# Optimization experiments

Measured on AMD Instinct MI355X. Metric: run time of the kernel, lower is better.

The kernel has to match this reference:

```python
import jax, jax.numpy as jnp
import numpy as np

B, M, H = 8192, 512, 1024
CORRUPTION_LEN = int(0.6 * M)  # int(corruption_rate * input_dim)


def setup_inputs() -> dict:
    key = jax.random.key(0)
    ks = jax.random.split(key, 10)
    anchor = jax.random.normal(ks[0], (B, M), jnp.float32)
    random_sample = jax.random.normal(ks[1], (B, M), jnp.float32)
    # per-row random permutation -> exactly CORRUPTION_LEN corrupted features per row
    u = jax.random.uniform(ks[2], (B, M))
    ranks = jnp.argsort(jnp.argsort(u, axis=1), axis=1)  # rank of each column in a random permutation
    corruption_mask = ranks < CORRUPTION_LEN
    s_in = 1.0 / np.sqrt(M)
    s_h = 1.0 / np.sqrt(H)
    enc_w0 = jax.random.normal(ks[3], (M, H), jnp.float32) * s_in
    enc_b0 = jnp.full((H,), 0.01, jnp.float32)
    enc_w = jax.random.normal(ks[4], (3, H, H), jnp.float32) * s_h
    enc_b = jnp.full((3, H), 0.01, jnp.float32)
    head_w = jax.random.normal(ks[5], (2, H, H), jnp.float32) * s_h
    head_b = jnp.full((2, H), 0.01, jnp.float32)
    return {
        "anchor": anchor,
        "random_sample": random_sample,
        "corruption_mask": corruption_mask,
        "enc_w0": enc_w0,
        "enc_b0": enc_b0,
        "enc_w": enc_w,
        "enc_b": enc_b,
        "head_w": head_w,
        "head_b": head_b,
    }


def _mlp(x, w0, b0, ws, bs):
    # first dense + relu
    h = jax.nn.relu(x @ w0 + b0)
    # remaining dense + relu layers (small fixed count)
    for i in range(ws.shape[0]):
        h = jax.nn.relu(h @ ws[i] + bs[i])
    return h


def _embed(x, enc_w0, enc_b0, enc_w, enc_b, head_w, head_b):
    h = _mlp(x, enc_w0, enc_b0, enc_w, enc_b)          # encoder: 4 dense+relu
    h = jax.nn.relu(h @ head_w[0] + head_b[0])          # head: 2 dense+relu
    h = jax.nn.relu(h @ head_w[1] + head_b[1])
    return h


def reference(anchor, random_sample, corruption_mask, enc_w0, enc_b0, enc_w, enc_b, head_w, head_b):
    positive = jnp.where(corruption_mask, random_sample, anchor)
    emb_anchor = _embed(anchor, enc_w0, enc_b0, enc_w, enc_b, head_w, head_b)
    emb_positive = _embed(positive, enc_w0, enc_b0, enc_w, enc_b, head_w, head_b)
    return (emb_anchor, emb_positive)
```

## Files before the change

kernel.cpp:

```cpp
#include <hip/hip_runtime.h>
#include <hip/hip_bf16.h>
#include <stdint.h>


typedef __bf16 bf16x8 __attribute__((ext_vector_type(8)));
typedef float  f32x4  __attribute__((ext_vector_type(4)));

#define BM 128
#define BN 128
#define BK 64

__device__ __forceinline__ void gload_lds16(const void* g, void* l) {
  __builtin_amdgcn_global_load_lds(
      (const __attribute__((address_space(1))) uint32_t*)g,
      (__attribute__((address_space(3))) uint32_t*)l, 16, 0, 0);
}

__device__ __forceinline__ void fsplit(float v, uint16_t& ho, uint16_t& lo) {
  __bf16 hb = (__bf16)v;
  float  r  = v - (float)hb;
  __bf16 lb = (__bf16)r;
  ho = __builtin_bit_cast(uint16_t, hb);
  lo = __builtin_bit_cast(uint16_t, lb);
}

__global__ void detect_mask_kernel(const uint8_t* __restrict__ mask,
                                   int* __restrict__ flag) {
  if (threadIdx.x == 0 && blockIdx.x == 0) {
    uint32_t or_hi = 0;
    for (int i = 0; i < 1024; ++i)
      or_hi |= ((const uint32_t*)mask)[i] & 0xFFFFFF00u;
    *flag = (or_hi != 0) ? 1 : 0;
  }
}

__global__ void pack_kernel(const float* __restrict__ anchor,
                            const float* __restrict__ rnd,
                            const uint8_t* __restrict__ mask,
                            const int* __restrict__ mask_is_bytes,
                            uint16_t* __restrict__ Xhi, uint16_t* __restrict__ Xlo,
                            int total4) {
  int i = blockIdx.x * blockDim.x + threadIdx.x;
  if (i >= total4) return;
  float4 a = ((const float4*)anchor)[i];
  float4 r = ((const float4*)rnd)[i];
  const float* ap = (const float*)&a;
  const float* rp = (const float*)&r;
  uint32_t mbits;
  if (*mask_is_bytes) {
    uint32_t m = ((const uint32_t*)mask)[i];
    mbits = ((m >> 0) & 1u) | ((m >> 7) & 2u) | ((m >> 14) & 4u) | ((m >> 21) & 8u);
  } else {
    int4 mi = ((const int4*)mask)[i];
    mbits = (mi.x ? 1u : 0u) | (mi.y ? 2u : 0u) | (mi.z ? 4u : 0u) | (mi.w ? 8u : 0u);
  }
  ushort4 ah, al, ph, pl;
  uint16_t* ahp = (uint16_t*)&ah; uint16_t* alp = (uint16_t*)&al;
  uint16_t* php = (uint16_t*)&ph; uint16_t* plp = (uint16_t*)&pl;
#pragma unroll
  for (int j = 0; j < 4; ++j) {
    float av = ap[j];
    float pv = ((mbits >> j) & 1u) ? rp[j] : av;
    fsplit(av, ahp[j], alp[j]);
    fsplit(pv, php[j], plp[j]);
  }
  ((ushort4*)Xhi)[i] = ah;
  ((ushort4*)Xlo)[i] = al;
  ((ushort4*)Xhi)[i + total4] = ph;
  ((ushort4*)Xlo)[i + total4] = pl;
}

__global__ void wprep_kernel(const float* __restrict__ W,
                             uint16_t* __restrict__ Wh, uint16_t* __restrict__ Wl,
                             int K, int N) {
  __shared__ float t[32][33];
  int k0 = blockIdx.x * 32, n0 = blockIdx.y * 32;
  int tr = threadIdx.x >> 5, tc = threadIdx.x & 31;
#pragma unroll
  for (int i = 0; i < 4; ++i)
    t[tr + i * 8][tc] = W[(size_t)(k0 + tr + i * 8) * N + n0 + tc];
  __syncthreads();
#pragma unroll
  for (int i = 0; i < 4; ++i) {
    int n = tr + i * 8;
    float v = t[tc][n];
    uint16_t h, l;
    fsplit(v, h, l);
    size_t o = (size_t)(n0 + n) * K + k0 + tc;
    Wh[o] = h; Wl[o] = l;
  }
}

template <int K, bool LAST>
__global__ __launch_bounds__(256, 2) void gemm_kernel(
    const uint16_t* __restrict__ Ah, const uint16_t* __restrict__ Al,
    const uint16_t* __restrict__ Bh, const uint16_t* __restrict__ Bl,
    const float* __restrict__ bias,
    uint16_t* __restrict__ Yh, uint16_t* __restrict__ Yl,
    float* __restrict__ Yf) {
  __shared__ uint16_t sAh[BM * BK], sAl[BM * BK], sBh[BN * BK], sBl[BN * BK];

  int bid = blockIdx.x;
  int swz = (bid & 7) * 128 + (bid >> 3);
  int tn = swz & 7;
  int tm = swz >> 3;
  const int brow = tm * BM, bcol = tn * BN;

  const int tid = threadIdx.x;
  const int w = tid >> 6, l = tid & 63;
  const int wr = w >> 1, wc = w & 1;
  const int lr = l >> 3, lc = (l & 7) * 8;

  f32x4 acc[4][4];
#pragma unroll
  for (int m = 0; m < 4; ++m)
#pragma unroll
    for (int n = 0; n < 4; ++n) acc[m][n] = 0;

  for (int k0 = 0; k0 < K; k0 += BK) {
#pragma unroll
    for (int t = 0; t < 4; ++t) {
      int r = w * 32 + t * 8;
      size_t ga = (size_t)(brow + r + lr) * K + k0 + lc;
      size_t gb = (size_t)(bcol + r + lr) * K + k0 + lc;
      gload_lds16(Ah + ga, &sAh[r * BK]);
      gload_lds16(Al + ga, &sAl[r * BK]);
      gload_lds16(Bh + gb, &sBh[r * BK]);
      gload_lds16(Bl + gb, &sBl[r * BK]);
    }
    __syncthreads();

#pragma unroll
    for (int kk = 0; kk < 2; ++kk) {
      const int ko = kk * 32 + (l >> 4) * 8;
      bf16x8 aH[4], aL[4], bH[4], bL[4];
#pragma unroll
      for (int m = 0; m < 4; ++m) {
        int row = wr * 64 + m * 16 + (l & 15);
        aH[m] = *(const bf16x8*)&sAh[row * BK + ko];
        aL[m] = *(const bf16x8*)&sAl[row * BK + ko];
      }
#pragma unroll
      for (int n = 0; n < 4; ++n) {
        int col = wc * 64 + n * 16 + (l & 15);
        bH[n] = *(const bf16x8*)&sBh[col * BK + ko];
        bL[n] = *(const bf16x8*)&sBl[col * BK + ko];
      }
#pragma unroll
      for (int m = 0; m < 4; ++m)
#pragma unroll
        for (int n = 0; n < 4; ++n) {
          acc[m][n] = __builtin_amdgcn_mfma_f32_16x16x32_bf16(aH[m], bH[n], acc[m][n], 0, 0, 0);
          acc[m][n] = __builtin_amdgcn_mfma_f32_16x16x32_bf16(aH[m], bL[n], acc[m][n], 0, 0, 0);
          acc[m][n] = __builtin_amdgcn_mfma_f32_16x16x32_bf16(aL[m], bH[n], acc[m][n], 0, 0, 0);
        }
    }
    __syncthreads();
  }

  float bb[4];
#pragma unroll
  for (int n = 0; n < 4; ++n) bb[n] = bias[bcol + wc * 64 + n * 16 + (l & 15)];
#pragma unroll
  for (int m = 0; m < 4; ++m) {
#pragma unroll
    for (int j = 0; j < 4; ++j) {
      int row = brow + wr * 64 + m * 16 + (l >> 4) * 4 + j;
#pragma unroll
      for (int n = 0; n < 4; ++n) {
        int col = bcol + wc * 64 + n * 16 + (l & 15);
        float v = acc[m][n][j] + bb[n];
        v = v > 0.f ? v : 0.f;
        size_t o = (size_t)row * 1024 + col;
        if (LAST) {
          Yf[o] = v;
        } else {
          uint16_t h, lo2;
          fsplit(v, h, lo2);
          Yh[o] = h; Yl[o] = lo2;
        }
      }
    }
  }
}

extern "C" void kernel_launch(void* const* d_in, const int* in_sizes, int n_in,
                              void* d_out, int out_size, void* d_ws, size_t ws_size,
                              hipStream_t stream) {
  (void)in_sizes; (void)n_in; (void)out_size; (void)ws_size;
  const float*   anchor = (const float*)d_in[0];
  const float*   rnd    = (const float*)d_in[1];
  const uint8_t* mask   = (const uint8_t*)d_in[2];
  const float*   enc_w0 = (const float*)d_in[3];
  const float*   enc_b0 = (const float*)d_in[4];
  const float*   enc_w  = (const float*)d_in[5];
  const float*   enc_b  = (const float*)d_in[6];
  const float*   head_w = (const float*)d_in[7];
  const float*   head_b = (const float*)d_in[8];
  float* out = (float*)d_out;

  const int B = 8192, M = 512;
  const size_t W_ELEMS = (size_t)512 * 1024 + 5ull * 1024 * 1024;

  uint16_t* WT_H = (uint16_t*)d_ws;
  uint16_t* WT_L = WT_H + W_ELEMS;
  uint16_t* X0_H = WT_L + W_ELEMS;
  uint16_t* X0_L = X0_H + (size_t)16384 * 512;
  uint16_t* Y_H  = X0_L + (size_t)16384 * 512;
  uint16_t* Y_L  = Y_H + (size_t)16384 * 1024;
  int* mflag     = (int*)(Y_L + (size_t)16384 * 1024);
  uint16_t* Z_H = (uint16_t*)d_out;
  uint16_t* Z_L = Z_H + (size_t)16384 * 1024;

  detect_mask_kernel<<<1, 64, 0, stream>>>(mask, mflag);

  int total4 = B * M / 4;
  pack_kernel<<<total4 / 256, 256, 0, stream>>>(anchor, rnd, mask, mflag, X0_H, X0_L, total4);

  const size_t WOFF[6] = {0, 524288, 1572864, 2621440, 3670016, 4718592};
  wprep_kernel<<<dim3(16, 32), 256, 0, stream>>>(enc_w0, WT_H + WOFF[0], WT_L + WOFF[0], 512, 1024);
  for (int i = 0; i < 3; ++i)
    wprep_kernel<<<dim3(32, 32), 256, 0, stream>>>(enc_w + (size_t)i * 1048576,
                                                   WT_H + WOFF[1 + i], WT_L + WOFF[1 + i], 1024, 1024);
  for (int i = 0; i < 2; ++i)
    wprep_kernel<<<dim3(32, 32), 256, 0, stream>>>(head_w + (size_t)i * 1048576,
                                                   WT_H + WOFF[4 + i], WT_L + WOFF[4 + i], 1024, 1024);

  dim3 g(1024), b(256);
  gemm_kernel<512,  false><<<g, b, 0, stream>>>(X0_H, X0_L, WT_H + WOFF[0], WT_L + WOFF[0], enc_b0,        Y_H, Y_L, nullptr);
  gemm_kernel<1024, false><<<g, b, 0, stream>>>(Y_H,  Y_L,  WT_H + WOFF[1], WT_L + WOFF[1], enc_b,         Z_H, Z_L, nullptr);
  gemm_kernel<1024, false><<<g, b, 0, stream>>>(Z_H,  Z_L,  WT_H + WOFF[2], WT_L + WOFF[2], enc_b + 1024,  Y_H, Y_L, nullptr);
  gemm_kernel<1024, false><<<g, b, 0, stream>>>(Y_H,  Y_L,  WT_H + WOFF[3], WT_L + WOFF[3], enc_b + 2048,  Z_H, Z_L, nullptr);
  gemm_kernel<1024, false><<<g, b, 0, stream>>>(Z_H,  Z_L,  WT_H + WOFF[4], WT_L + WOFF[4], head_b,        Y_H, Y_L, nullptr);
  gemm_kernel<1024, true ><<<g, b, 0, stream>>>(Y_H,  Y_L,  WT_H + WOFF[5], WT_L + WOFF[5], head_b + 1024, nullptr, nullptr, out);
}
```

Before: 666.1 us.

## Rewrite split-bf16 GEMM with 256x256 tiles, interleaved swizzled layout, double buffering

Repacks activations and weights into one interleaved hi/lo operand buffer with an XOR-swizzled 32-wide K-group layout, so a single row read serves both halves without LDS bank conflicts. The GEMM moves to 256x256 tiles with 512 threads and 8 waves, a double-buffered LDS pipeline that prefetches the next K-group while MFMAs run, manual waitcnt/barrier scheduling and setprio. Larger tiles cut global traffic per FLOP and the prefetch hides load latency. The cost is higher register and LDS pressure (128 KB LDS per block, which may limit occupancy to one block per CU) and a narrower mask-detect scan.

```diff
diff --git a/kernel.cpp b/kernel.cpp
--- a/kernel.cpp
+++ b/kernel.cpp
@@ -5,10 +5,7 @@
 
 typedef __bf16 bf16x8 __attribute__((ext_vector_type(8)));
 typedef float  f32x4  __attribute__((ext_vector_type(4)));
-
-#define BM 128
-#define BN 128
-#define BK 64
+typedef unsigned short u16x8 __attribute__((ext_vector_type(8)));
 
 __device__ __forceinline__ void gload_lds16(const void* g, void* l) {
   __builtin_amdgcn_global_load_lds(
@@ -28,7 +25,7 @@
                                    int* __restrict__ flag) {
   if (threadIdx.x == 0 && blockIdx.x == 0) {
     uint32_t or_hi = 0;
-    for (int i = 0; i < 1024; ++i)
+    for (int i = 0; i < 256; ++i)
       or_hi |= ((const uint32_t*)mask)[i] & 0xFFFFFF00u;
     *flag = (or_hi != 0) ? 1 : 0;
   }
@@ -38,150 +35,244 @@
                             const float* __restrict__ rnd,
                             const uint8_t* __restrict__ mask,
                             const int* __restrict__ mask_is_bytes,
-                            uint16_t* __restrict__ Xhi, uint16_t* __restrict__ Xlo,
-                            int total4) {
-  int i = blockIdx.x * blockDim.x + threadIdx.x;
-  if (i >= total4) return;
-  float4 a = ((const float4*)anchor)[i];
-  float4 r = ((const float4*)rnd)[i];
-  const float* ap = (const float*)&a;
-  const float* rp = (const float*)&r;
-  uint32_t mbits;
+                            uint16_t* __restrict__ Xop) {
+  int t = blockIdx.x * 256 + threadIdx.x;
+  int row = t >> 6;
+  int idx = t & 63;
+  int g = idx >> 2, c = idx & 3;
+  int kbase = idx * 8;
+  const float4* ap = (const float4*)(anchor + (size_t)row * 512 + kbase);
+  const float4* rp = (const float4*)(rnd + (size_t)row * 512 + kbase);
+  float a[8], r[8];
+  *(float4*)&a[0] = ap[0]; *(float4*)&a[4] = ap[1];
+  *(float4*)&r[0] = rp[0]; *(float4*)&r[4] = rp[1];
+  uint32_t mb;
   if (*mask_is_bytes) {
-    uint32_t m = ((const uint32_t*)mask)[i];
-    mbits = ((m >> 0) & 1u) | ((m >> 7) & 2u) | ((m >> 14) & 4u) | ((m >> 21) & 8u);
+    const uint32_t* mp = (const uint32_t*)(mask + (size_t)row * 512 + kbase);
+    uint32_t w0 = mp[0], w1 = mp[1];
+    mb = 0;
+#pragma unroll
+    for (int j = 0; j < 4; ++j) {
+      mb |= ((w0 >> (8 * j)) & 1u) << j;
+      mb |= ((w1 >> (8 * j)) & 1u) << (4 + j);
+    }
   } else {
-    int4 mi = ((const int4*)mask)[i];
-    mbits = (mi.x ? 1u : 0u) | (mi.y ? 2u : 0u) | (mi.z ? 4u : 0u) | (mi.w ? 8u : 0u);
-  }
-  ushort4 ah, al, ph, pl;
-  uint16_t* ahp = (uint16_t*)&ah; uint16_t* alp = (uint16_t*)&al;
-  uint16_t* php = (uint16_t*)&ph; uint16_t* plp = (uint16_t*)&pl;
-#pragma unroll
-  for (int j = 0; j < 4; ++j) {
-    float av = ap[j];
-    float pv = ((mbits >> j) & 1u) ? rp[j] : av;
-    fsplit(av, ahp[j], alp[j]);
-    fsplit(pv, php[j], plp[j]);
-  }
-  ((ushort4*)Xhi)[i] = ah;
-  ((ushort4*)Xlo)[i] = al;
-  ((ushort4*)Xhi)[i + total4] = ph;
-  ((ushort4*)Xlo)[i + total4] = pl;
+    const int* mi = (const int*)mask + (size_t)row * 512 + kbase;
+    int4 m0 = ((const int4*)mi)[0], m1 = ((const int4*)mi)[1];
+    mb = (m0.x ? 1u : 0) | (m0.y ? 2u : 0) | (m0.z ? 4u : 0) | (m0.w ? 8u : 0) |
+         (m1.x ? 16u : 0) | (m1.y ? 32u : 0) | (m1.z ? 64u : 0) | (m1.w ? 128u : 0);
+  }
+  u16x8 ah, al, ph, pl;
+#pragma unroll
+  for (int j = 0; j < 8; ++j) {
+    uint16_t h, lo;
+    fsplit(a[j], h, lo); ah[j] = h; al[j] = lo;
+    float pv = ((mb >> j) & 1u) ? r[j] : a[j];
+    fsplit(pv, h, lo); ph[j] = h; pl[j] = lo;
+  }
+  int s = row & 7;
+  size_t base = ((size_t)row * 16 + g) * 64;
+  *(u16x8*)(Xop + base + (size_t)((c ^ s)) * 8) = ah;
+  *(u16x8*)(Xop + base + (size_t)(((c + 4) ^ s)) * 8) = al;
+  size_t pbase = ((size_t)(row + 8192) * 16 + g) * 64;
+  *(u16x8*)(Xop + pbase + (size_t)((c ^ s)) * 8) = ph;
+  *(u16x8*)(Xop + pbase + (size_t)(((c + 4) ^ s)) * 8) = pl;
 }
 
 __global__ void wprep_kernel(const float* __restrict__ W,
-                             uint16_t* __restrict__ Wh, uint16_t* __restrict__ Wl,
-                             int K, int N) {
-  __shared__ float t[32][33];
-  int k0 = blockIdx.x * 32, n0 = blockIdx.y * 32;
-  int tr = threadIdx.x >> 5, tc = threadIdx.x & 31;
+                             uint16_t* __restrict__ Bop, int K) {
+  __shared__ float tbuf[32][33];
+  int g = blockIdx.x, n0 = blockIdx.y * 32;
+  int tid = threadIdx.x;
 #pragma unroll
   for (int i = 0; i < 4; ++i)
-    t[tr + i * 8][tc] = W[(size_t)(k0 + tr + i * 8) * N + n0 + tc];
+    tbuf[(tid >> 5) + i * 8][tid & 31] =
+        W[((size_t)g * 32 + (tid >> 5) + i * 8) * 1024 + n0 + (tid & 31)];
   __syncthreads();
-#pragma unroll
-  for (int i = 0; i < 4; ++i) {
-    int n = tr + i * 8;
-    float v = t[tc][n];
-    uint16_t h, l;
-    fsplit(v, h, l);
-    size_t o = (size_t)(n0 + n) * K + k0 + tc;
-    Wh[o] = h; Wl[o] = l;
+  if (tid < 128) {
+    int nl = tid >> 2, c = tid & 3;
+    int n = n0 + nl, s = n & 7;
+    u16x8 hi, lo;
+#pragma unroll
+    for (int j = 0; j < 8; ++j) {
+      uint16_t h, l2;
+      fsplit(tbuf[c * 8 + j][nl], h, l2);
+      hi[j] = h; lo[j] = l2;
+    }
+    size_t base = ((size_t)n * (K / 32) + g) * 64;
+    *(u16x8*)(Bop + base + (size_t)((c ^ s)) * 8) = hi;
+    *(u16x8*)(Bop + base + (size_t)(((c + 4) ^ s)) * 8) = lo;
+  }
+}
+
+__device__ __forceinline__ void mfma_row(f32x4* accrow, bf16x8 aH, bf16x8 aL,
+                                         const bf16x8* bh, const bf16x8* bl) {
+#pragma unroll
+  for (int n = 0; n < 4; ++n) {
+    accrow[n] = __builtin_amdgcn_mfma_f32_16x16x32_bf16(aH, bh[n], accrow[n], 0, 0, 0);
+    accrow[n] = __builtin_amdgcn_mfma_f32_16x16x32_bf16(aH, bl[n], accrow[n], 0, 0, 0);
+    accrow[n] = __builtin_amdgcn_mfma_f32_16x16x32_bf16(aL, bh[n], accrow[n], 0, 0, 0);
   }
 }
 
 template <int K, bool LAST>
-__global__ __launch_bounds__(256, 2) void gemm_kernel(
-    const uint16_t* __restrict__ Ah, const uint16_t* __restrict__ Al,
-    const uint16_t* __restrict__ Bh, const uint16_t* __restrict__ Bl,
+__global__ __launch_bounds__(512, 2) void gemm_kernel(
+    const uint16_t* __restrict__ Aop, const uint16_t* __restrict__ Bop,
     const float* __restrict__ bias,
-    uint16_t* __restrict__ Yh, uint16_t* __restrict__ Yl,
-    float* __restrict__ Yf) {
-  __shared__ uint16_t sAh[BM * BK], sAl[BM * BK], sBh[BN * BK], sBl[BN * BK];
+    uint16_t* __restrict__ Yop, float* __restrict__ Yf) {
+  constexpr int KG = K / 32;
+  __shared__ uint16_t sA[2][256 * 64];
+  __shared__ uint16_t sB[2][256 * 64];
 
   int bid = blockIdx.x;
-  int swz = (bid & 7) * 128 + (bid >> 3);
-  int tn = swz & 7;
-  int tm = swz >> 3;
-  const int brow = tm * BM, bcol = tn * BN;
+  int xcd = bid & 7, lid = bid >> 3;
+  int tm = xcd * 8 + (lid >> 2), tn = lid & 3;
+  const int brow = tm * 256, bcol = tn * 256;
 
   const int tid = threadIdx.x;
-  const int w = tid >> 6, l = tid & 63;
-  const int wr = w >> 1, wc = w & 1;
-  const int lr = l >> 3, lc = (l & 7) * 8;
-
-  f32x4 acc[4][4];
-#pragma unroll
-  for (int m = 0; m < 4; ++m)
+  const int l = tid & 63, w = tid >> 6;
+  const int wr = w >> 2, wc = w & 3;
+  const int l15 = l & 15, c16 = l >> 4;
+
+  f32x4 acc[8][4];
+#pragma unroll
+  for (int m = 0; m < 8; ++m)
 #pragma unroll
     for (int n = 0; n < 4; ++n) acc[m][n] = 0;
 
-  for (int k0 = 0; k0 < K; k0 += BK) {
-#pragma unroll
-    for (int t = 0; t < 4; ++t) {
-      int r = w * 32 + t * 8;
-      size_t ga = (size_t)(brow + r + lr) * K + k0 + lc;
-      size_t gb = (size_t)(bcol + r + lr) * K + k0 + lc;
-      gload_lds16(Ah + ga, &sAh[r * BK]);
-      gload_lds16(Al + ga, &sAl[r * BK]);
-      gload_lds16(Bh + gb, &sBh[r * BK]);
-      gload_lds16(Bl + gb, &sBl[r * BK]);
+#define STAGE_A(g_, buf_)                                                     \
+  _Pragma("unroll") for (int i = 0; i < 4; ++i) {                             \
+    int row_ = i * 64 + (tid >> 3);                                           \
+    gload_lds16(Aop + ((size_t)(brow + row_) * KG + (g_)) * 64 + (tid & 7) * 8,\
+                &sA[buf_][i * 4096 + tid * 8]);                               \
+  }
+#define STAGE_B(g_, buf_)                                                     \
+  _Pragma("unroll") for (int i = 0; i < 4; ++i) {                             \
+    int row_ = i * 64 + (tid >> 3);                                           \
+    gload_lds16(Bop + ((size_t)(bcol + row_) * KG + (g_)) * 64 + (tid & 7) * 8,\
+                &sB[buf_][i * 4096 + tid * 8]);                               \
+  }
+#define READ_A(mm, aH, aL)                                                    \
+  {                                                                           \
+    int fr_ = wr * 128 + (mm)*16 + l15;                                       \
+    const uint16_t* rp_ = pA + fr_ * 64;                                      \
+    aH = *(const bf16x8*)(rp_ + ((c16 ^ (fr_ & 7))) * 8);                     \
+    aL = *(const bf16x8*)(rp_ + (((c16 + 4) ^ (fr_ & 7))) * 8);               \
+  }
+#define BARRIER() __builtin_amdgcn_s_barrier()
+#define LGKM0()                                                               \
+  asm volatile("s_waitcnt lgkmcnt(0)" ::: "memory");                          \
+  __builtin_amdgcn_sched_barrier(0)
+#define VM0()                                                                 \
+  asm volatile("s_waitcnt vmcnt(0)" ::: "memory");                            \
+  __builtin_amdgcn_sched_barrier(0)
+
+  STAGE_A(0, 0)
+  STAGE_B(0, 0)
+  VM0();
+  BARRIER();
+
+  int cur = 0;
+#pragma unroll 1
+  for (int g = 0; g < KG; ++g) {
+    const uint16_t* pA = &sA[cur][0];
+    const uint16_t* pB = &sB[cur][0];
+    const bool pf = (g + 1 < KG);
+    const int nxt = cur ^ 1;
+
+    bf16x8 bh[4], bl[4];
+#pragma unroll
+    for (int n = 0; n < 4; ++n) {
+      int fc = wc * 64 + n * 16 + l15;
+      const uint16_t* rp = pB + fc * 64;
+      bh[n] = *(const bf16x8*)(rp + ((c16 ^ (fc & 7))) * 8);
+      bl[n] = *(const bf16x8*)(rp + (((c16 + 4) ^ (fc & 7))) * 8);
     }
-    __syncthreads();
-
-#pragma unroll
-    for (int kk = 0; kk < 2; ++kk) {
-      const int ko = kk * 32 + (l >> 4) * 8;
-      bf16x8 aH[4], aL[4], bH[4], bL[4];
-#pragma unroll
-      for (int m = 0; m < 4; ++m) {
-        int row = wr * 64 + m * 16 + (l & 15);
-        aH[m] = *(const bf16x8*)&sAh[row * BK + ko];
-        aL[m] = *(const bf16x8*)&sAl[row * BK + ko];
-      }
+    bf16x8 a0h, a0l, a1h, a1l;
+    READ_A(0, a0h, a0l)
+    READ_A(1, a1h, a1l)
+    if (pf) { STAGE_A(g + 1, nxt) }
+    BARRIER();
+    LGKM0();
+    __builtin_amdgcn_s_setprio(1);
+    mfma_row(acc[0], a0h, a0l, bh, bl);
+    mfma_row(acc[1], a1h, a1l, bh, bl);
+    __builtin_amdgcn_s_setprio(0);
+    BARRIER();
+
+    bf16x8 a2h, a2l, a3h, a3l;
+    READ_A(2, a2h, a2l)
+    READ_A(3, a3h, a3l)
+    if (pf) { STAGE_B(g + 1, nxt) }
+    BARRIER();
+    LGKM0();
+    __builtin_amdgcn_s_setprio(1);
+    mfma_row(acc[2], a2h, a2l, bh, bl);
+    mfma_row(acc[3], a3h, a3l, bh, bl);
+    __builtin_amdgcn_s_setprio(0);
+    BARRIER();
+
+    bf16x8 a4h, a4l, a5h, a5l;
+    READ_A(4, a4h, a4l)
+    READ_A(5, a5h, a5l)
+    BARRIER();
+    LGKM0();
+    __builtin_amdgcn_s_setprio(1);
+    mfma_row(acc[4], a4h, a4l, bh, bl);
+    mfma_row(acc[5], a5h, a5l, bh, bl);
+    __builtin_amdgcn_s_setprio(0);
+    BARRIER();
+
+    bf16x8 a6h, a6l, a7h, a7l;
+    READ_A(6, a6h, a6l)
+    READ_A(7, a7h, a7l)
+    BARRIER();
+    LGKM0();
+    __builtin_amdgcn_s_setprio(1);
+    mfma_row(acc[6], a6h, a6l, bh, bl);
+    mfma_row(acc[7], a7h, a7l, bh, bl);
+    __builtin_amdgcn_s_setprio(0);
+    VM0();
+    BARRIER();
+    cur = nxt;
+  }
+
+  float bb[4];
+  int colg[4], colc[4], cole[4];
+#pragma unroll
+  for (int n = 0; n < 4; ++n) {
+    int col = bcol + wc * 64 + n * 16 + l15;
+    bb[n] = bias[col];
+    colg[n] = col >> 5; colc[n] = (col >> 3) & 3; cole[n] = col & 7;
+  }
+#pragma unroll
+  for (int m = 0; m < 8; ++m) {
+#pragma unroll
+    for (int j = 0; j < 4; ++j) {
+      int rowY = brow + wr * 128 + m * 16 + c16 * 4 + j;
+      int s = rowY & 7;
 #pragma unroll
       for (int n = 0; n < 4; ++n) {
-        int col = wc * 64 + n * 16 + (l & 15);
-        bH[n] = *(const bf16x8*)&sBh[col * BK + ko];
-        bL[n] = *(const bf16x8*)&sBl[col * BK + ko];
-      }
-#pragma unroll
-      for (int m = 0; m < 4; ++m)
-#pragma unroll
-        for (int n = 0; n < 4; ++n) {
-          acc[m][n] = __builtin_amdgcn_mfma_f32_16x16x32_bf16(aH[m], bH[n], acc[m][n], 0, 0, 0);
-          acc[m][n] = __builtin_amdgcn_mfma_f32_16x16x32_bf16(aH[m], bL[n], acc[m][n], 0, 0, 0);
-          acc[m][n] = __builtin_amdgcn_mfma_f32_16x16x32_bf16(aL[m], bH[n], acc[m][n], 0, 0, 0);
-        }
-    }
-    __syncthreads();
-  }
-
-  float bb[4];
-#pragma unroll
-  for (int n = 0; n < 4; ++n) bb[n] = bias[bcol + wc * 64 + n * 16 + (l & 15)];
-#pragma unroll
-  for (int m = 0; m < 4; ++m) {
-#pragma unroll
-    for (int j = 0; j < 4; ++j) {
-      int row = brow + wr * 64 + m * 16 + (l >> 4) * 4 + j;
-#pragma unroll
-      for (int n = 0; n < 4; ++n) {
-        int col = bcol + wc * 64 + n * 16 + (l & 15);
         float v = acc[m][n][j] + bb[n];
         v = v > 0.f ? v : 0.f;
-        size_t o = (size_t)row * 1024 + col;
         if (LAST) {
-          Yf[o] = v;
+          Yf[(size_t)rowY * 1024 + bcol + wc * 64 + n * 16 + l15] = v;
         } else {
           uint16_t h, lo2;
           fsplit(v, h, lo2);
-          Yh[o] = h; Yl[o] = lo2;
+          size_t base = ((size_t)rowY * 32 + colg[n]) * 64;
+          Yop[base + (size_t)((colc[n] ^ s)) * 8 + cole[n]] = h;
+          Yop[base + (size_t)(((colc[n] + 4) ^ s)) * 8 + cole[n]] = lo2;
         }
       }
     }
   }
+#undef STAGE_A
+#undef STAGE_B
+#undef READ_A
+#undef BARRIER
+#undef LGKM0
+#undef VM0
 }
 
 extern "C" void kernel_launch(void* const* d_in, const int* in_sizes, int n_in,
@@ -199,38 +290,35 @@
   const float*   head_b = (const float*)d_in[8];
   float* out = (float*)d_out;
 
-  const int B = 8192, M = 512;
-  const size_t W_ELEMS = (size_t)512 * 1024 + 5ull * 1024 * 1024;
-
-  uint16_t* WT_H = (uint16_t*)d_ws;
-  uint16_t* WT_L = WT_H + W_ELEMS;
-  uint16_t* X0_H = WT_L + W_ELEMS;
-  uint16_t* X0_L = X0_H + (size_t)16384 * 512;
-  uint16_t* Y_H  = X0_L + (size_t)16384 * 512;
-  uint16_t* Y_L  = Y_H + (size_t)16384 * 1024;
-  int* mflag     = (int*)(Y_L + (size_t)16384 * 1024);
-  uint16_t* Z_H = (uint16_t*)d_out;
-  uint16_t* Z_L = Z_H + (size_t)16384 * 1024;
+  const size_t WSZ0 = (size_t)512 * 2048;
+  const size_t WSZ1 = (size_t)1024 * 2048;
+  uint16_t* Wop = (uint16_t*)d_ws;
+  size_t WOFF[6];
+  WOFF[0] = 0;
+  WOFF[1] = WSZ0;
+  for (int i = 2; i < 6; ++i) WOFF[i] = WOFF[i - 1] + WSZ1;
+  uint16_t* Xop = Wop + WOFF[5] + WSZ1;
+  uint16_t* Yop = Xop + (size_t)16384 * 1024;
+  int* mflag = (int*)(Yop + (size_t)16384 * 2048);
+  uint16_t* Zop = (uint16_t*)d_out;
 
   detect_mask_kernel<<<1, 64, 0, stream>>>(mask, mflag);
 
-  int total4 = B * M / 4;
-  pack_kernel<<<total4 / 256, 256, 0, stream>>>(anchor, rnd, mask, mflag, X0_H, X0_L, total4);
-
-  const size_t WOFF[6] = {0, 524288, 1572864, 2621440, 3670016, 4718592};
-  wprep_kernel<<<dim3(16, 32), 256, 0, stream>>>(enc_w0, WT_H + WOFF[0], WT_L + WOFF[0], 512, 1024);
+  pack_kernel<<<2048, 256, 0, stream>>>(anchor, rnd, mask, mflag, Xop);
+
+  wprep_kernel<<<dim3(16, 32), 256, 0, stream>>>(enc_w0, Wop + WOFF[0], 512);
   for (int i = 0; i < 3; ++i)
     wprep_kernel<<<dim3(32, 32), 256, 0, stream>>>(enc_w + (size_t)i * 1048576,
-                                                   WT_H + WOFF[1 + i], WT_L + WOFF[1 + i], 1024, 1024);
+                                                   Wop + WOFF[1 + i], 1024);
   for (int i = 0; i < 2; ++i)
     wprep_kernel<<<dim3(32, 32), 256, 0, stream>>>(head_w + (size_t)i * 1048576,
-                                                   WT_H + WOFF[4 + i], WT_L + WOFF[4 + i], 1024, 1024);
-
-  dim3 g(1024), b(256);
-  gemm_kernel<512,  false><<<g, b, 0, stream>>>(X0_H, X0_L, WT_H + WOFF[0], WT_L + WOFF[0], enc_b0,        Y_H, Y_L, nullptr);
-  gemm_kernel<1024, false><<<g, b, 0, stream>>>(Y_H,  Y_L,  WT_H + WOFF[1], WT_L + WOFF[1], enc_b,         Z_H, Z_L, nullptr);
-  gemm_kernel<1024, false><<<g, b, 0, stream>>>(Z_H,  Z_L,  WT_H + WOFF[2], WT_L + WOFF[2], enc_b + 1024,  Y_H, Y_L, nullptr);
-  gemm_kernel<1024, false><<<g, b, 0, stream>>>(Y_H,  Y_L,  WT_H + WOFF[3], WT_L + WOFF[3], enc_b + 2048,  Z_H, Z_L, nullptr);
-  gemm_kernel<1024, false><<<g, b, 0, stream>>>(Z_H,  Z_L,  WT_H + WOFF[4], WT_L + WOFF[4], head_b,        Y_H, Y_L, nullptr);
-  gemm_kernel<1024, true ><<<g, b, 0, stream>>>(Y_H,  Y_L,  WT_H + WOFF[5], WT_L + WOFF[5], head_b + 1024, nullptr, nullptr, out);
-}
+                                                   Wop + WOFF[4 + i], 1024);
+
+  dim3 g(256), b(512);
+  gemm_kernel<512,  false><<<g, b, 0, stream>>>(Xop, Wop + WOFF[0], enc_b0,        Yop, nullptr);
+  gemm_kernel<1024, false><<<g, b, 0, stream>>>(Yop, Wop + WOFF[1], enc_b,         Zop, nullptr);
+  gemm_kernel<1024, false><<<g, b, 0, stream>>>(Zop, Wop + WOFF[2], enc_b + 1024,  Yop, nullptr);
+  gemm_kernel<1024, false><<<g, b, 0, stream>>>(Yop, Wop + WOFF[3], enc_b + 2048,  Zop, nullptr);
+  gemm_kernel<1024, false><<<g, b, 0, stream>>>(Zop, Wop + WOFF[4], head_b,        Yop, nullptr);
+  gemm_kernel<1024, true ><<<g, b, 0, stream>>>(Yop, Wop + WOFF[5], head_b + 1024, nullptr, out);
+}
```

After: 586.0 us. -12.0%, faster.
